# Kernel tuning notes

Hardware: AMD Instinct MI355X
Metric: run time of the kernel (lower is better)

## Reference

```python
import jax, jax.numpy as jnp
import numpy as np

D_MODEL = 1024
N_HEADS = 16
HEAD_DIM = D_MODEL // N_HEADS


def setup_inputs() -> dict:
    key = jax.random.key(0)
    k1, k2, k3 = jax.random.split(key, 3)
    x = jax.random.normal(k1, (4, 2048, D_MODEL), dtype=jnp.float32)
    # torch Linear(d, 3d, bias=False): y = x @ W.T with W [3d, d]; store transposed [d, 3d]
    s = 1.0 / np.sqrt(D_MODEL)
    w_qkv = jax.random.uniform(k2, (D_MODEL, 3 * D_MODEL), dtype=jnp.float32, minval=-s, maxval=s)
    w_proj = jax.random.uniform(k3, (D_MODEL, D_MODEL), dtype=jnp.float32, minval=-s, maxval=s)
    return {"x": x, "w_qkv": w_qkv, "w_proj": w_proj}


def reference(x, w_qkv, w_proj):
    B, T, D = x.shape
    qkv = (x @ w_qkv).reshape(B, T, 3, N_HEADS, HEAD_DIM)
    qkv = jnp.transpose(qkv, (2, 0, 3, 1, 4))  # [3, B, H, T, hd]
    q, k, v = qkv[0], qkv[1], qkv[2]
    # NOTE: original module applies NO 1/sqrt(head_dim) scaling
    attn = jax.nn.softmax(jnp.einsum('bhqd,bhkd->bhqk', q, k), axis=-1)
    out = jnp.einsum('bhqk,bhkd->bhqd', attn, v)
    out = jnp.transpose(out, (0, 2, 1, 3)).reshape(B, T, D)
    return out @ w_proj
```

## Files before the change

kernel.cpp:

```cpp
#include <hip/hip_runtime.h>

typedef __bf16 bf16;
typedef __bf16 bf16x8 __attribute__((ext_vector_type(8)));
typedef float f32x4 __attribute__((ext_vector_type(4)));
typedef unsigned int uint;
typedef unsigned short ushort;

typedef const __attribute__((address_space(1))) void* gas_ptr;
typedef __attribute__((address_space(3))) void* las_ptr;

__device__ __forceinline__ void load16_lds(const void* g, void* l) {
  __builtin_amdgcn_global_load_lds((gas_ptr)g, (las_ptr)l, 16, 0, 0);
}

__global__ __launch_bounds__(256) void cast_f32_bf16(
    const float* __restrict__ in, bf16* __restrict__ out) {
  size_t i = (size_t)blockIdx.x * 256 + threadIdx.x;
  const float4* p = reinterpret_cast<const float4*>(in) + i * 2;
  float4 a = p[0], b = p[1];
  bf16x8 v;
  v[0] = (bf16)a.x; v[1] = (bf16)a.y; v[2] = (bf16)a.z; v[3] = (bf16)a.w;
  v[4] = (bf16)b.x; v[5] = (bf16)b.y; v[6] = (bf16)b.z; v[7] = (bf16)b.w;
  reinterpret_cast<bf16x8*>(out)[i] = v;
}

__global__ __launch_bounds__(256) void transpose_f32_bf16(
    const float* __restrict__ in, bf16* __restrict__ out, int K, int N) {
  __shared__ __attribute__((aligned(16))) bf16 tile[64 * 72];
  const int k0 = blockIdx.y * 64, n0 = blockIdx.x * 64;
  const int tid = threadIdx.x;
  for (int c = tid; c < 1024; c += 256) {
    int ki = c >> 4, j4 = c & 15;
    float4 f = *reinterpret_cast<const float4*>(in + (size_t)(k0 + ki) * N + n0 + j4 * 4);
    bf16* t = &tile[ki * 72 + j4 * 4];
    t[0] = (bf16)f.x; t[1] = (bf16)f.y; t[2] = (bf16)f.z; t[3] = (bf16)f.w;
  }
  __syncthreads();
  for (int c = tid; c < 512; c += 256) {
    int ni = c >> 3, k8 = c & 7;
    bf16x8 v;
    for (int j = 0; j < 8; j++) v[j] = tile[(k8 * 8 + j) * 72 + ni];
    *reinterpret_cast<bf16x8*>(out + (size_t)(n0 + ni) * K + k0 + k8 * 8) = v;
  }
}

template <typename CT>
__global__ __launch_bounds__(256, 2) void gemm_lds(
    const bf16* __restrict__ A, const bf16* __restrict__ Bt,
    CT* __restrict__ C, int M, int N, int K) {
  __shared__ __attribute__((aligned(16))) bf16 As[128 * 64];
  __shared__ __attribute__((aligned(16))) bf16 Bs[128 * 64];
  const int tid = threadIdx.x;
  const int wave = tid >> 6;
  const int lane = tid & 63;
  const int l15 = lane & 15;
  const int quad = lane >> 4;
  const int nwg = gridDim.x * gridDim.y;
  const int orig = blockIdx.y * gridDim.x + blockIdx.x;
  const int swz = (orig & 7) * (nwg >> 3) + (orig >> 3);
  const int m0 = (swz / gridDim.x) * 128;
  const int n0 = (swz % gridDim.x) * 128;
  const int wm = (wave >> 1) * 64;
  const int wn = (wave & 1) * 64;

  f32x4 acc[4][4] = {};

  for (int kt = 0; kt < K; kt += 64) {
    __syncthreads();
    for (int it = 0; it < 4; ++it) {
      int p = it * 256 + wave * 64 + lane;
      int row = p >> 3, kc = (p & 7) ^ (row & 7);
      load16_lds(A + (size_t)(m0 + row) * K + kt + kc * 8, &As[p * 8]);
      load16_lds(Bt + (size_t)(n0 + row) * K + kt + kc * 8, &Bs[p * 8]);
    }
    __syncthreads();
    for (int kk = 0; kk < 64; kk += 32) {
      const int kc = (kk >> 3) + quad;
      bf16x8 af[4], bfr[4];
      for (int i = 0; i < 4; i++) {
        int row = wm + i * 16 + l15;
        af[i] = *reinterpret_cast<const bf16x8*>(&As[(row * 8 + (kc ^ (row & 7))) * 8]);
      }
      for (int j = 0; j < 4; j++) {
        int row = wn + j * 16 + l15;
        bfr[j] = *reinterpret_cast<const bf16x8*>(&Bs[(row * 8 + (kc ^ (row & 7))) * 8]);
      }
      for (int i = 0; i < 4; i++)
        for (int j = 0; j < 4; j++)
          acc[i][j] = __builtin_amdgcn_mfma_f32_16x16x32_bf16(af[i], bfr[j], acc[i][j], 0, 0, 0);
    }
  }

  for (int i = 0; i < 4; i++)
    for (int j = 0; j < 4; j++)
      for (int r = 0; r < 4; r++) {
        int row = m0 + wm + i * 16 + quad * 4 + r;
        int col = n0 + wn + j * 16 + l15;
        C[(size_t)row * N + col] = (CT)acc[i][j][r];
      }
}

__device__ __forceinline__ int vs_dw(int d, int kdw) {
  return d * 32 + (kdw ^ ((((d >> 3) ^ d) & 7) * 4));
}

__global__ __launch_bounds__(512, 4) void attn_kernel(
    const bf16* __restrict__ qkv, bf16* __restrict__ out) {
  __shared__ __attribute__((aligned(16))) bf16 Ks[2][64 * 64];
  __shared__ __attribute__((aligned(16))) uint Vs[2][64 * 32];

  const int tid = threadIdx.x;
  const int wave = tid >> 6;
  const int lane = tid & 63;
  const int l15 = lane & 15;
  const int quad = lane >> 4;
  const int b = blockIdx.x >> 4;
  const int h = blockIdx.x & 15;
  const int qt0 = blockIdx.y * 128;
  const bf16* base = qkv + (size_t)b * 2048 * 3072 + h * 64;
  const float L2E = 1.44269504f;

  bf16x8 aq0, aq1;
  {
    const bf16* qrow = base + (size_t)(qt0 + wave * 16 + l15) * 3072;
    aq0 = *reinterpret_cast<const bf16x8*>(qrow + quad * 8);
    aq1 = *reinterpret_cast<const bf16x8*>(qrow + 32 + quad * 8);
    for (int j = 0; j < 8; j++) {
      aq0[j] = (bf16)((float)aq0[j] * L2E);
      aq1[j] = (bf16)((float)aq1[j] * L2E);
    }
  }

  bf16x8 bones = {};
  if (l15 == 0)
    for (int j = 0; j < 8; j++) bones[j] = (bf16)1.0f;

  float m_q = -1e30f;
  f32x4 o[4] = {};
  f32x4 l_acc = {};

  const int t2 = tid & 255;
  const int kp = t2 >> 3;
  const int oct = t2 & 7;
  const bool vrole = (wave < 4);
  const int prow = ((kp & 4) << 2) | ((kp & 24) >> 1) | (kp & 3);
  const int kxor = oct ^ (prow & 7);
  const int kdst0 = (prow * 8 + kxor) * 8;
  const int kdst1 = kdst0 + 32 * 64;

  bf16x8 pre0, pre1;
  if (vrole) {
    const bf16* v0p = base + (size_t)(2 * kp) * 3072 + 2048 + oct * 8;
    pre0 = *reinterpret_cast<const bf16x8*>(v0p);
    pre1 = *reinterpret_cast<const bf16x8*>(v0p + 3072);
  } else {
    const bf16* kb = base + 1024 + (size_t)kp * 3072 + oct * 8;
    pre0 = *reinterpret_cast<const bf16x8*>(kb);
    pre1 = *reinterpret_cast<const bf16x8*>(kb + (size_t)32 * 3072);
  }

  for (int kt = 0; kt < 2048; kt += 64) {
    const int cur = (kt >> 6) & 1;
    if (vrole) {
      const ushort* u0 = reinterpret_cast<const ushort*>(&pre0);
      const ushort* u1 = reinterpret_cast<const ushort*>(&pre1);
      for (int i = 0; i < 8; i++)
        Vs[cur][vs_dw(oct * 8 + i, kp)] = (uint)u0[i] | ((uint)u1[i] << 16);
    } else {
      *reinterpret_cast<bf16x8*>(&Ks[cur][kdst0]) = pre0;
      *reinterpret_cast<bf16x8*>(&Ks[cur][kdst1]) = pre1;
    }
    __syncthreads();

    if (kt + 64 < 2048) {
      const bf16* nb = base + (size_t)(kt + 64) * 3072;
      if (vrole) {
        const bf16* v0p = nb + (size_t)(2 * kp) * 3072 + 2048 + oct * 8;
        pre0 = *reinterpret_cast<const bf16x8*>(v0p);
        pre1 = *reinterpret_cast<const bf16x8*>(v0p + 3072);
      } else {
        const bf16* kb = nb + 1024 + (size_t)kp * 3072 + oct * 8;
        pre0 = *reinterpret_cast<const bf16x8*>(kb);
        pre1 = *reinterpret_cast<const bf16x8*>(kb + (size_t)32 * 3072);
      }
    }

    f32x4 s[4];
    __builtin_amdgcn_s_setprio(1);
    for (int n = 0; n < 4; n++) {
      int row = n * 16 + l15;
      int xr = row & 7;
      bf16x8 ak0 = *reinterpret_cast<const bf16x8*>(&Ks[cur][(row * 8 + (quad ^ xr)) * 8]);
      bf16x8 ak1 = *reinterpret_cast<const bf16x8*>(&Ks[cur][(row * 8 + ((4 + quad) ^ xr)) * 8]);
      f32x4 z = {};
      z = __builtin_amdgcn_mfma_f32_16x16x32_bf16(ak0, aq0, z, 0, 0, 0);
      z = __builtin_amdgcn_mfma_f32_16x16x32_bf16(ak1, aq1, z, 0, 0, 0);
      s[n] = z;
    }
    __builtin_amdgcn_s_setprio(0);

    float mt = fmaxf(fmaxf(s[0][0], s[0][1]), s[0][2]);
    mt = fmaxf(fmaxf(mt, s[0][3]), s[1][0]);
    mt = fmaxf(fmaxf(mt, s[1][1]), s[1][2]);
    mt = fmaxf(fmaxf(mt, s[1][3]), s[2][0]);
    mt = fmaxf(fmaxf(mt, s[2][1]), s[2][2]);
    mt = fmaxf(fmaxf(mt, s[2][3]), s[3][0]);
    mt = fmaxf(fmaxf(mt, s[3][1]), s[3][2]);
    mt = fmaxf(mt, s[3][3]);
    mt = fmaxf(mt, __shfl_xor(mt, 16, 64));
    mt = fmaxf(mt, __shfl_xor(mt, 32, 64));

    if (!__all(mt - m_q <= 8.0f)) {
      float mn = fmaxf(m_q, mt);
      float alpha = __builtin_amdgcn_exp2f(m_q - mn);
      m_q = mn;
      float a0 = __shfl(alpha, quad * 4 + 0, 64);
      float a1 = __shfl(alpha, quad * 4 + 1, 64);
      float a2 = __shfl(alpha, quad * 4 + 2, 64);
      float a3 = __shfl(alpha, quad * 4 + 3, 64);
      l_acc[0] *= a0; l_acc[1] *= a1; l_acc[2] *= a2; l_acc[3] *= a3;
      for (int n = 0; n < 4; n++) {
        o[n][0] *= a0; o[n][1] *= a1; o[n][2] *= a2; o[n][3] *= a3;
      }
    }

    bf16x8 ap0, ap1;
    for (int r = 0; r < 4; r++) {
      ap0[r]     = (bf16)__builtin_amdgcn_exp2f(s[0][r] - m_q);
      ap0[4 + r] = (bf16)__builtin_amdgcn_exp2f(s[1][r] - m_q);
      ap1[r]     = (bf16)__builtin_amdgcn_exp2f(s[2][r] - m_q);
      ap1[4 + r] = (bf16)__builtin_amdgcn_exp2f(s[3][r] - m_q);
    }

    __builtin_amdgcn_s_setprio(1);
    l_acc = __builtin_amdgcn_mfma_f32_16x16x32_bf16(ap0, bones, l_acc, 0, 0, 0);
    l_acc = __builtin_amdgcn_mfma_f32_16x16x32_bf16(ap1, bones, l_acc, 0, 0, 0);

    for (int n = 0; n < 4; n++) {
      int d = n * 16 + l15;
      uint4 u0 = *reinterpret_cast<const uint4*>(&Vs[cur][vs_dw(d, quad * 4)]);
      uint4 u1 = *reinterpret_cast<const uint4*>(&Vs[cur][vs_dw(d, 16 + quad * 4)]);
      bf16x8 bv0 = *reinterpret_cast<const bf16x8*>(&u0);
      bf16x8 bv1 = *reinterpret_cast<const bf16x8*>(&u1);
      o[n] = __builtin_amdgcn_mfma_f32_16x16x32_bf16(ap0, bv0, o[n], 0, 0, 0);
      o[n] = __builtin_amdgcn_mfma_f32_16x16x32_bf16(ap1, bv1, o[n], 0, 0, 0);
    }
    __builtin_amdgcn_s_setprio(0);
  }

  for (int r = 0; r < 4; r++) {
    float lv = __shfl(l_acc[r], quad * 16, 64);
    float inv = 1.0f / lv;
    int q = qt0 + wave * 16 + quad * 4 + r;
    bf16* orow = out + (size_t)(b * 2048 + q) * 1024 + h * 64;
    for (int n = 0; n < 4; n++) orow[n * 16 + l15] = (bf16)(o[n][r] * inv);
  }
}

extern "C" void kernel_launch(void* const* d_in, const int* in_sizes, int n_in,
                              void* d_out, int out_size, void* d_ws, size_t ws_size,
                              hipStream_t stream) {
  const float* x = (const float*)d_in[0];
  const float* w_qkv = (const float*)d_in[1];
  const float* w_proj = (const float*)d_in[2];
  float* out = (float*)d_out;

  bf16* ws = (bf16*)d_ws;
  bf16* x_bf = ws;
  bf16* wqkvT = x_bf + (size_t)8192 * 1024;
  bf16* wprojT = wqkvT + 3072 * 1024;
  bf16* qkv = wprojT + 1024 * 1024;
  bf16* attn_out = qkv + (size_t)8192 * 3072;

  cast_f32_bf16<<<4096, 256, 0, stream>>>(x, x_bf);
  transpose_f32_bf16<<<dim3(48, 16), 256, 0, stream>>>(w_qkv, wqkvT, 1024, 3072);
  transpose_f32_bf16<<<dim3(16, 16), 256, 0, stream>>>(w_proj, wprojT, 1024, 1024);
  gemm_lds<bf16><<<dim3(24, 64), 256, 0, stream>>>(x_bf, wqkvT, qkv, 8192, 3072, 1024);
  attn_kernel<<<dim3(64, 16), 512, 0, stream>>>(qkv, attn_out);
  gemm_lds<float><<<dim3(8, 64), 256, 0, stream>>>(attn_out, wprojT, out, 8192, 1024, 1024);
}
```

Before: 276.4 us.

## Process two query tiles per wave in attention and load K via direct-to-LDS

Each wave now handles two 16-row query blocks (256 queries per workgroup), so every K/V tile staged in LDS is reused twice and the grid halves. K tiles are fetched with global_load_lds straight into shared memory instead of passing through registers. The V staging load is spread across all 512 threads using 4-element vectors. The cost is roughly double the accumulator register pressure, with occupancy hints lowered from 4 to 2 blocks, and half as many workgroups to fill the GPU.

```diff
diff --git a/kernel.cpp b/kernel.cpp
--- a/kernel.cpp
+++ b/kernel.cpp
@@ -2,6 +2,7 @@
 
 typedef __bf16 bf16;
 typedef __bf16 bf16x8 __attribute__((ext_vector_type(8)));
+typedef __bf16 bf16x4 __attribute__((ext_vector_type(4)));
 typedef float f32x4 __attribute__((ext_vector_type(4)));
 typedef unsigned int uint;
 typedef unsigned short ushort;
@@ -104,7 +105,7 @@
   return d * 32 + (kdw ^ ((((d >> 3) ^ d) & 7) * 4));
 }
 
-__global__ __launch_bounds__(512, 4) void attn_kernel(
+__global__ __launch_bounds__(512, 2) void attn_kernel(
     const bf16* __restrict__ qkv, bf16* __restrict__ out) {
   __shared__ __attribute__((aligned(16))) bf16 Ks[2][64 * 64];
   __shared__ __attribute__((aligned(16))) uint Vs[2][64 * 32];
@@ -116,18 +117,23 @@
   const int quad = lane >> 4;
   const int b = blockIdx.x >> 4;
   const int h = blockIdx.x & 15;
-  const int qt0 = blockIdx.y * 128;
+  const int qt0 = blockIdx.y * 256;
   const bf16* base = qkv + (size_t)b * 2048 * 3072 + h * 64;
   const float L2E = 1.44269504f;
 
-  bf16x8 aq0, aq1;
+  bf16x8 aqA0, aqA1, aqB0, aqB1;
   {
-    const bf16* qrow = base + (size_t)(qt0 + wave * 16 + l15) * 3072;
-    aq0 = *reinterpret_cast<const bf16x8*>(qrow + quad * 8);
-    aq1 = *reinterpret_cast<const bf16x8*>(qrow + 32 + quad * 8);
+    const bf16* qa = base + (size_t)(qt0 + wave * 16 + l15) * 3072;
+    const bf16* qb = qa + (size_t)128 * 3072;
+    aqA0 = *reinterpret_cast<const bf16x8*>(qa + quad * 8);
+    aqA1 = *reinterpret_cast<const bf16x8*>(qa + 32 + quad * 8);
+    aqB0 = *reinterpret_cast<const bf16x8*>(qb + quad * 8);
+    aqB1 = *reinterpret_cast<const bf16x8*>(qb + 32 + quad * 8);
     for (int j = 0; j < 8; j++) {
-      aq0[j] = (bf16)((float)aq0[j] * L2E);
-      aq1[j] = (bf16)((float)aq1[j] * L2E);
+      aqA0[j] = (bf16)((float)aqA0[j] * L2E);
+      aqA1[j] = (bf16)((float)aqA1[j] * L2E);
+      aqB0[j] = (bf16)((float)aqB0[j] * L2E);
+      aqB1[j] = (bf16)((float)aqB1[j] * L2E);
     }
   }
 
@@ -135,57 +141,43 @@
   if (l15 == 0)
     for (int j = 0; j < 8; j++) bones[j] = (bf16)1.0f;
 
-  float m_q = -1e30f;
-  f32x4 o[4] = {};
-  f32x4 l_acc = {};
-
-  const int t2 = tid & 255;
-  const int kp = t2 >> 3;
-  const int oct = t2 & 7;
-  const bool vrole = (wave < 4);
-  const int prow = ((kp & 4) << 2) | ((kp & 24) >> 1) | (kp & 3);
-  const int kxor = oct ^ (prow & 7);
-  const int kdst0 = (prow * 8 + kxor) * 8;
-  const int kdst1 = kdst0 + 32 * 64;
-
-  bf16x8 pre0, pre1;
-  if (vrole) {
-    const bf16* v0p = base + (size_t)(2 * kp) * 3072 + 2048 + oct * 8;
-    pre0 = *reinterpret_cast<const bf16x8*>(v0p);
-    pre1 = *reinterpret_cast<const bf16x8*>(v0p + 3072);
-  } else {
-    const bf16* kb = base + 1024 + (size_t)kp * 3072 + oct * 8;
-    pre0 = *reinterpret_cast<const bf16x8*>(kb);
-    pre1 = *reinterpret_cast<const bf16x8*>(kb + (size_t)32 * 3072);
-  }
+  float mA = -1e30f, mB = -1e30f;
+  f32x4 oA[4] = {}, oB[4] = {};
+  f32x4 lA = {}, lB = {};
+
+  const int c = tid;
+  const int krow = c >> 3;
+  const int kc8 = (c & 7) ^ (krow & 7);
+  const int ktrue = (((krow >> 4) & 1) << 2) | (((krow >> 3) & 1) << 4) |
+                    (((krow >> 2) & 1) << 3) | (krow & 3) | (krow & 32);
+  const bf16* kgp = base + 1024 + (size_t)ktrue * 3072 + kc8 * 8;
+
+  const int vkp = tid >> 4;
+  const int vd0 = (tid & 15) * 4;
+  const bf16* vgp = base + (size_t)(2 * vkp) * 3072 + 2048 + vd0;
+
+  load16_lds(kgp, &Ks[0][c * 8]);
+  bf16x4 vpre0 = *reinterpret_cast<const bf16x4*>(vgp);
+  bf16x4 vpre1 = *reinterpret_cast<const bf16x4*>(vgp + 3072);
 
   for (int kt = 0; kt < 2048; kt += 64) {
     const int cur = (kt >> 6) & 1;
-    if (vrole) {
-      const ushort* u0 = reinterpret_cast<const ushort*>(&pre0);
-      const ushort* u1 = reinterpret_cast<const ushort*>(&pre1);
-      for (int i = 0; i < 8; i++)
-        Vs[cur][vs_dw(oct * 8 + i, kp)] = (uint)u0[i] | ((uint)u1[i] << 16);
-    } else {
-      *reinterpret_cast<bf16x8*>(&Ks[cur][kdst0]) = pre0;
-      *reinterpret_cast<bf16x8*>(&Ks[cur][kdst1]) = pre1;
+    {
+      const ushort* u0 = reinterpret_cast<const ushort*>(&vpre0);
+      const ushort* u1 = reinterpret_cast<const ushort*>(&vpre1);
+      for (int i = 0; i < 4; i++)
+        Vs[cur][vs_dw(vd0 + i, vkp)] = (uint)u0[i] | ((uint)u1[i] << 16);
     }
     __syncthreads();
 
     if (kt + 64 < 2048) {
-      const bf16* nb = base + (size_t)(kt + 64) * 3072;
-      if (vrole) {
-        const bf16* v0p = nb + (size_t)(2 * kp) * 3072 + 2048 + oct * 8;
-        pre0 = *reinterpret_cast<const bf16x8*>(v0p);
-        pre1 = *reinterpret_cast<const bf16x8*>(v0p + 3072);
-      } else {
-        const bf16* kb = nb + 1024 + (size_t)kp * 3072 + oct * 8;
-        pre0 = *reinterpret_cast<const bf16x8*>(kb);
-        pre1 = *reinterpret_cast<const bf16x8*>(kb + (size_t)32 * 3072);
-      }
-    }
-
-    f32x4 s[4];
+      const size_t off = (size_t)(kt + 64) * 3072;
+      load16_lds(kgp + off, &Ks[cur ^ 1][c * 8]);
+      vpre0 = *reinterpret_cast<const bf16x4*>(vgp + off);
+      vpre1 = *reinterpret_cast<const bf16x4*>(vgp + off + 3072);
+    }
+
+    f32x4 sA[4], sB[4];
     __builtin_amdgcn_s_setprio(1);
     for (int n = 0; n < 4; n++) {
       int row = n * 16 + l15;
@@ -193,67 +185,120 @@
       bf16x8 ak0 = *reinterpret_cast<const bf16x8*>(&Ks[cur][(row * 8 + (quad ^ xr)) * 8]);
       bf16x8 ak1 = *reinterpret_cast<const bf16x8*>(&Ks[cur][(row * 8 + ((4 + quad) ^ xr)) * 8]);
       f32x4 z = {};
-      z = __builtin_amdgcn_mfma_f32_16x16x32_bf16(ak0, aq0, z, 0, 0, 0);
-      z = __builtin_amdgcn_mfma_f32_16x16x32_bf16(ak1, aq1, z, 0, 0, 0);
-      s[n] = z;
+      z = __builtin_amdgcn_mfma_f32_16x16x32_bf16(ak0, aqA0, z, 0, 0, 0);
+      z = __builtin_amdgcn_mfma_f32_16x16x32_bf16(ak1, aqA1, z, 0, 0, 0);
+      sA[n] = z;
+      f32x4 w = {};
+      w = __builtin_amdgcn_mfma_f32_16x16x32_bf16(ak0, aqB0, w, 0, 0, 0);
+      w = __builtin_amdgcn_mfma_f32_16x16x32_bf16(ak1, aqB1, w, 0, 0, 0);
+      sB[n] = w;
     }
     __builtin_amdgcn_s_setprio(0);
 
-    float mt = fmaxf(fmaxf(s[0][0], s[0][1]), s[0][2]);
-    mt = fmaxf(fmaxf(mt, s[0][3]), s[1][0]);
-    mt = fmaxf(fmaxf(mt, s[1][1]), s[1][2]);
-    mt = fmaxf(fmaxf(mt, s[1][3]), s[2][0]);
-    mt = fmaxf(fmaxf(mt, s[2][1]), s[2][2]);
-    mt = fmaxf(fmaxf(mt, s[2][3]), s[3][0]);
-    mt = fmaxf(fmaxf(mt, s[3][1]), s[3][2]);
-    mt = fmaxf(mt, s[3][3]);
-    mt = fmaxf(mt, __shfl_xor(mt, 16, 64));
-    mt = fmaxf(mt, __shfl_xor(mt, 32, 64));
-
-    if (!__all(mt - m_q <= 8.0f)) {
-      float mn = fmaxf(m_q, mt);
-      float alpha = __builtin_amdgcn_exp2f(m_q - mn);
-      m_q = mn;
-      float a0 = __shfl(alpha, quad * 4 + 0, 64);
-      float a1 = __shfl(alpha, quad * 4 + 1, 64);
-      float a2 = __shfl(alpha, quad * 4 + 2, 64);
-      float a3 = __shfl(alpha, quad * 4 + 3, 64);
-      l_acc[0] *= a0; l_acc[1] *= a1; l_acc[2] *= a2; l_acc[3] *= a3;
+    {
+      float mt = fmaxf(fmaxf(sA[0][0], sA[0][1]), sA[0][2]);
+      mt = fmaxf(fmaxf(mt, sA[0][3]), sA[1][0]);
+      mt = fmaxf(fmaxf(mt, sA[1][1]), sA[1][2]);
+      mt = fmaxf(fmaxf(mt, sA[1][3]), sA[2][0]);
+      mt = fmaxf(fmaxf(mt, sA[2][1]), sA[2][2]);
+      mt = fmaxf(fmaxf(mt, sA[2][3]), sA[3][0]);
+      mt = fmaxf(fmaxf(mt, sA[3][1]), sA[3][2]);
+      mt = fmaxf(mt, sA[3][3]);
+      mt = fmaxf(mt, __shfl_xor(mt, 16, 64));
+      mt = fmaxf(mt, __shfl_xor(mt, 32, 64));
+      if (!__all(mt - mA <= 8.0f)) {
+        float mn = fmaxf(mA, mt);
+        float alpha = __builtin_amdgcn_exp2f(mA - mn);
+        mA = mn;
+        float a0 = __shfl(alpha, quad * 4 + 0, 64);
+        float a1 = __shfl(alpha, quad * 4 + 1, 64);
+        float a2 = __shfl(alpha, quad * 4 + 2, 64);
+        float a3 = __shfl(alpha, quad * 4 + 3, 64);
+        lA[0] *= a0; lA[1] *= a1; lA[2] *= a2; lA[3] *= a3;
+        for (int n = 0; n < 4; n++) {
+          oA[n][0] *= a0; oA[n][1] *= a1; oA[n][2] *= a2; oA[n][3] *= a3;
+        }
+      }
+      bf16x8 ap0, ap1;
+      for (int r = 0; r < 4; r++) {
+        ap0[r]     = (bf16)__builtin_amdgcn_exp2f(sA[0][r] - mA);
+        ap0[4 + r] = (bf16)__builtin_amdgcn_exp2f(sA[1][r] - mA);
+        ap1[r]     = (bf16)__builtin_amdgcn_exp2f(sA[2][r] - mA);
+        ap1[4 + r] = (bf16)__builtin_amdgcn_exp2f(sA[3][r] - mA);
+      }
+      __builtin_amdgcn_s_setprio(1);
+      lA = __builtin_amdgcn_mfma_f32_16x16x32_bf16(ap0, bones, lA, 0, 0, 0);
+      lA = __builtin_amdgcn_mfma_f32_16x16x32_bf16(ap1, bones, lA, 0, 0, 0);
       for (int n = 0; n < 4; n++) {
-        o[n][0] *= a0; o[n][1] *= a1; o[n][2] *= a2; o[n][3] *= a3;
-      }
-    }
-
-    bf16x8 ap0, ap1;
-    for (int r = 0; r < 4; r++) {
-      ap0[r]     = (bf16)__builtin_amdgcn_exp2f(s[0][r] - m_q);
-      ap0[4 + r] = (bf16)__builtin_amdgcn_exp2f(s[1][r] - m_q);
-      ap1[r]     = (bf16)__builtin_amdgcn_exp2f(s[2][r] - m_q);
-      ap1[4 + r] = (bf16)__builtin_amdgcn_exp2f(s[3][r] - m_q);
-    }
-
-    __builtin_amdgcn_s_setprio(1);
-    l_acc = __builtin_amdgcn_mfma_f32_16x16x32_bf16(ap0, bones, l_acc, 0, 0, 0);
-    l_acc = __builtin_amdgcn_mfma_f32_16x16x32_bf16(ap1, bones, l_acc, 0, 0, 0);
-
-    for (int n = 0; n < 4; n++) {
-      int d = n * 16 + l15;
-      uint4 u0 = *reinterpret_cast<const uint4*>(&Vs[cur][vs_dw(d, quad * 4)]);
-      uint4 u1 = *reinterpret_cast<const uint4*>(&Vs[cur][vs_dw(d, 16 + quad * 4)]);
-      bf16x8 bv0 = *reinterpret_cast<const bf16x8*>(&u0);
-      bf16x8 bv1 = *reinterpret_cast<const bf16x8*>(&u1);
-      o[n] = __builtin_amdgcn_mfma_f32_16x16x32_bf16(ap0, bv0, o[n], 0, 0, 0);
-      o[n] = __builtin_amdgcn_mfma_f32_16x16x32_bf16(ap1, bv1, o[n], 0, 0, 0);
-    }
-    __builtin_amdgcn_s_setprio(0);
+        int d = n * 16 + l15;
+        uint4 u0 = *reinterpret_cast<const uint4*>(&Vs[cur][vs_dw(d, quad * 4)]);
+        uint4 u1 = *reinterpret_cast<const uint4*>(&Vs[cur][vs_dw(d, 16 + quad * 4)]);
+        bf16x8 bv0 = *reinterpret_cast<const bf16x8*>(&u0);
+        bf16x8 bv1 = *reinterpret_cast<const bf16x8*>(&u1);
+        oA[n] = __builtin_amdgcn_mfma_f32_16x16x32_bf16(ap0, bv0, oA[n], 0, 0, 0);
+        oA[n] = __builtin_amdgcn_mfma_f32_16x16x32_bf16(ap1, bv1, oA[n], 0, 0, 0);
+      }
+      __builtin_amdgcn_s_setprio(0);
+    }
+
+    {
+      float mt = fmaxf(fmaxf(sB[0][0], sB[0][1]), sB[0][2]);
+      mt = fmaxf(fmaxf(mt, sB[0][3]), sB[1][0]);
+      mt = fmaxf(fmaxf(mt, sB[1][1]), sB[1][2]);
+      mt = fmaxf(fmaxf(mt, sB[1][3]), sB[2][0]);
+      mt = fmaxf(fmaxf(mt, sB[2][1]), sB[2][2]);
+      mt = fmaxf(fmaxf(mt, sB[2][3]), sB[3][0]);
+      mt = fmaxf(fmaxf(mt, sB[3][1]), sB[3][2]);
+      mt = fmaxf(mt, sB[3][3]);
+      mt = fmaxf(mt, __shfl_xor(mt, 16, 64));
+      mt = fmaxf(mt, __shfl_xor(mt, 32, 64));
+      if (!__all(mt - mB <= 8.0f)) {
+        float mn = fmaxf(mB, mt);
+        float alpha = __builtin_amdgcn_exp2f(mB - mn);
+        mB = mn;
+        float a0 = __shfl(alpha, quad * 4 + 0, 64);
+        float a1 = __shfl(alpha, quad * 4 + 1, 64);
+        float a2 = __shfl(alpha, quad * 4 + 2, 64);
+        float a3 = __shfl(alpha, quad * 4 + 3, 64);
+        lB[0] *= a0; lB[1] *= a1; lB[2] *= a2; lB[3] *= a3;
+        for (int n = 0; n < 4; n++) {
+          oB[n][0] *= a0; oB[n][1] *= a1; oB[n][2] *= a2; oB[n][3] *= a3;
+        }
+      }
+      bf16x8 ap0, ap1;
+      for (int r = 0; r < 4; r++) {
+        ap0[r]     = (bf16)__builtin_amdgcn_exp2f(sB[0][r] - mB);
+        ap0[4 + r] = (bf16)__builtin_amdgcn_exp2f(sB[1][r] - mB);
+        ap1[r]     = (bf16)__builtin_amdgcn_exp2f(sB[2][r] - mB);
+        ap1[4 + r] = (bf16)__builtin_amdgcn_exp2f(sB[3][r] - mB);
+      }
+      __builtin_amdgcn_s_setprio(1);
+      lB = __builtin_amdgcn_mfma_f32_16x16x32_bf16(ap0, bones, lB, 0, 0, 0);
+      lB = __builtin_amdgcn_mfma_f32_16x16x32_bf16(ap1, bones, lB, 0, 0, 0);
+      for (int n = 0; n < 4; n++) {
+        int d = n * 16 + l15;
+        uint4 u0 = *reinterpret_cast<const uint4*>(&Vs[cur][vs_dw(d, quad * 4)]);
+        uint4 u1 = *reinterpret_cast<const uint4*>(&Vs[cur][vs_dw(d, 16 + quad * 4)]);
+        bf16x8 bv0 = *reinterpret_cast<const bf16x8*>(&u0);
+        bf16x8 bv1 = *reinterpret_cast<const bf16x8*>(&u1);
+        oB[n] = __builtin_amdgcn_mfma_f32_16x16x32_bf16(ap0, bv0, oB[n], 0, 0, 0);
+        oB[n] = __builtin_amdgcn_mfma_f32_16x16x32_bf16(ap1, bv1, oB[n], 0, 0, 0);
+      }
+      __builtin_amdgcn_s_setprio(0);
+    }
   }
 
   for (int r = 0; r < 4; r++) {
-    float lv = __shfl(l_acc[r], quad * 16, 64);
-    float inv = 1.0f / lv;
-    int q = qt0 + wave * 16 + quad * 4 + r;
-    bf16* orow = out + (size_t)(b * 2048 + q) * 1024 + h * 64;
-    for (int n = 0; n < 4; n++) orow[n * 16 + l15] = (bf16)(o[n][r] * inv);
+    float lvA = __shfl(lA[r], quad * 16, 64);
+    float invA = 1.0f / lvA;
+    int qA = qt0 + wave * 16 + quad * 4 + r;
+    bf16* orowA = out + (size_t)(b * 2048 + qA) * 1024 + h * 64;
+    for (int n = 0; n < 4; n++) orowA[n * 16 + l15] = (bf16)(oA[n][r] * invA);
+
+    float lvB = __shfl(lB[r], quad * 16, 64);
+    float invB = 1.0f / lvB;
+    bf16* orowB = orowA + (size_t)128 * 1024;
+    for (int n = 0; n < 4; n++) orowB[n * 16 + l15] = (bf16)(oB[n][r] * invB);
   }
 }
 
@@ -276,6 +321,6 @@
   transpose_f32_bf16<<<dim3(48, 16), 256, 0, stream>>>(w_qkv, wqkvT, 1024, 3072);
   transpose_f32_bf16<<<dim3(16, 16), 256, 0, stream>>>(w_proj, wprojT, 1024, 1024);
   gemm_lds<bf16><<<dim3(24, 64), 256, 0, stream>>>(x_bf, wqkvT, qkv, 8192, 3072, 1024);
-  attn_kernel<<<dim3(64, 16), 512, 0, stream>>>(qkv, attn_out);
+  attn_kernel<<<dim3(64, 8), 512, 0, stream>>>(qkv, attn_out);
   gemm_lds<float><<<dim3(8, 64), 256, 0, stream>>>(attn_out, wprojT, out, 8192, 1024, 1024);
 }
```

After: 284.9 us. 3.1% more time.

## Use 256x128 GEMM tiles with 512 threads and triple-buffered LDS prefetch

Applied to the files above, without the earlier changes.

Both GEMMs now use a 256x128 output tile computed by 8 waves instead of a 128x128 tile with 4 waves. The K loop gains a three-stage LDS ring filled by global_load_lds, with an explicit vmcnt wait and a single barrier per iteration, so global loads run two tiles ahead of compute. MFMA sections are wrapped in s_setprio. The larger tile cuts B-tile reloads and the grid size. In exchange, LDS use rises to about 144KB per block, which limits occupancy, and the hand-written waitcnt values assume a fixed count of outstanding loads.

```diff
diff --git a/kernel.cpp b/kernel.cpp
--- a/kernel.cpp
+++ b/kernel.cpp
@@ -45,11 +45,11 @@
 }
 
 template <typename CT>
-__global__ __launch_bounds__(256, 2) void gemm_lds(
+__global__ __launch_bounds__(512, 2) void gemm_256(
     const bf16* __restrict__ A, const bf16* __restrict__ Bt,
     CT* __restrict__ C, int M, int N, int K) {
-  __shared__ __attribute__((aligned(16))) bf16 As[128 * 64];
-  __shared__ __attribute__((aligned(16))) bf16 Bs[128 * 64];
+  __shared__ __attribute__((aligned(16))) bf16 As[3][256 * 64];
+  __shared__ __attribute__((aligned(16))) bf16 Bs[3][128 * 64];
   const int tid = threadIdx.x;
   const int wave = tid >> 6;
   const int lane = tid & 63;
@@ -58,36 +58,59 @@
   const int nwg = gridDim.x * gridDim.y;
   const int orig = blockIdx.y * gridDim.x + blockIdx.x;
   const int swz = (orig & 7) * (nwg >> 3) + (orig >> 3);
-  const int m0 = (swz / gridDim.x) * 128;
+  const int m0 = (swz / gridDim.x) * 256;
   const int n0 = (swz % gridDim.x) * 128;
   const int wm = (wave >> 1) * 64;
   const int wn = (wave & 1) * 64;
 
   f32x4 acc[4][4] = {};
-
-  for (int kt = 0; kt < K; kt += 64) {
-    __syncthreads();
+  const int nt = K >> 6;
+
+  auto stage = [&](int kt, int b) {
     for (int it = 0; it < 4; ++it) {
-      int p = it * 256 + wave * 64 + lane;
+      int p = it * 512 + tid;
       int row = p >> 3, kc = (p & 7) ^ (row & 7);
-      load16_lds(A + (size_t)(m0 + row) * K + kt + kc * 8, &As[p * 8]);
-      load16_lds(Bt + (size_t)(n0 + row) * K + kt + kc * 8, &Bs[p * 8]);
-    }
-    __syncthreads();
-    for (int kk = 0; kk < 64; kk += 32) {
-      const int kc = (kk >> 3) + quad;
+      load16_lds(A + (size_t)(m0 + row) * K + kt + kc * 8, &As[b][p * 8]);
+    }
+    for (int it = 0; it < 2; ++it) {
+      int p = it * 512 + tid;
+      int row = p >> 3, kc = (p & 7) ^ (row & 7);
+      load16_lds(Bt + (size_t)(n0 + row) * K + kt + kc * 8, &Bs[b][p * 8]);
+    }
+  };
+
+  stage(0, 0);
+  if (nt > 1) stage(64, 1);
+
+  for (int t = 0; t < nt; ++t) {
+    const int cur = t % 3;
+    if (t + 1 < nt) {
+      asm volatile("s_waitcnt vmcnt(6)" ::: "memory");
+    } else {
+      asm volatile("s_waitcnt vmcnt(0)" ::: "memory");
+    }
+    asm volatile("s_barrier" ::: "memory");
+
+    if (t + 2 < nt) stage((t + 2) << 6, (t + 2) % 3);
+
+    const bf16* Ab = &As[cur][0];
+    const bf16* Bb = &Bs[cur][0];
+    for (int kk = 0; kk < 2; ++kk) {
+      const int kc = kk * 4 + quad;
       bf16x8 af[4], bfr[4];
       for (int i = 0; i < 4; i++) {
         int row = wm + i * 16 + l15;
-        af[i] = *reinterpret_cast<const bf16x8*>(&As[(row * 8 + (kc ^ (row & 7))) * 8]);
+        af[i] = *reinterpret_cast<const bf16x8*>(&Ab[(row * 8 + (kc ^ (row & 7))) * 8]);
       }
       for (int j = 0; j < 4; j++) {
         int row = wn + j * 16 + l15;
-        bfr[j] = *reinterpret_cast<const bf16x8*>(&Bs[(row * 8 + (kc ^ (row & 7))) * 8]);
-      }
+        bfr[j] = *reinterpret_cast<const bf16x8*>(&Bb[(row * 8 + (kc ^ (row & 7))) * 8]);
+      }
+      __builtin_amdgcn_s_setprio(1);
       for (int i = 0; i < 4; i++)
         for (int j = 0; j < 4; j++)
           acc[i][j] = __builtin_amdgcn_mfma_f32_16x16x32_bf16(af[i], bfr[j], acc[i][j], 0, 0, 0);
+      __builtin_amdgcn_s_setprio(0);
     }
   }
 
@@ -275,7 +298,7 @@
   cast_f32_bf16<<<4096, 256, 0, stream>>>(x, x_bf);
   transpose_f32_bf16<<<dim3(48, 16), 256, 0, stream>>>(w_qkv, wqkvT, 1024, 3072);
   transpose_f32_bf16<<<dim3(16, 16), 256, 0, stream>>>(w_proj, wprojT, 1024, 1024);
-  gemm_lds<bf16><<<dim3(24, 64), 256, 0, stream>>>(x_bf, wqkvT, qkv, 8192, 3072, 1024);
+  gemm_256<bf16><<<dim3(24, 32), 512, 0, stream>>>(x_bf, wqkvT, qkv, 8192, 3072, 1024);
   attn_kernel<<<dim3(64, 16), 512, 0, stream>>>(qkv, attn_out);
-  gemm_lds<float><<<dim3(8, 64), 256, 0, stream>>>(attn_out, wprojT, out, 8192, 1024, 1024);
-}
+  gemm_256<float><<<dim3(8, 32), 512, 0, stream>>>(attn_out, wprojT, out, 8192, 1024, 1024);
+}
```

Result: slower. 289.5 us (+4.7%).
